# Kernel tuning notes

Hardware: AMD Instinct MI355X
Metric: run time of the kernel (lower is better)

The kernel has to match this reference:

```python
import jax, jax.numpy as jnp
import numpy as np

B, N, C = 2, 10000, 128
NH, NP = 4, 20          # n_heads, n_points (n_levels = 1)
DH = C // NH            # head dim = 32
HW = 100                # spatial shape (100, 100), N = HW*HW


def setup_inputs() -> dict:
    key = jax.random.key(0)
    ks = jax.random.split(key, 12)
    s = 0.05  # small param scale so softmax/linears stay well-conditioned
    return {
        "query": jax.random.normal(ks[0], (B, N, C), jnp.float32),
        "query_pos": jax.random.normal(ks[1], (B, N, C), jnp.float32),
        "W_val": jax.random.normal(ks[2], (C, C), jnp.float32) * s,
        "b_val": jax.random.normal(ks[3], (C,), jnp.float32) * s,
        "W_off": jax.random.normal(ks[4], (NH * NP * 2, C), jnp.float32) * s,
        "b_off": jax.random.normal(ks[5], (NH * NP * 2,), jnp.float32) * s,
        "W_attn": jax.random.normal(ks[6], (NH * NP, C), jnp.float32) * s,
        "b_attn": jax.random.normal(ks[7], (NH * NP,), jnp.float32) * s,
        "W_out1": jax.random.normal(ks[8], (C, C), jnp.float32) * s,
        "b_out1": jax.random.normal(ks[9], (C,), jnp.float32) * s,
        "W_out2": jax.random.normal(ks[10], (C, C), jnp.float32) * s,
        "b_out2": jax.random.normal(ks[11], (C,), jnp.float32) * s,
    }


def _msdeform_forward(query, query_pos, W_val, b_val, W_off, b_off,
                      W_attn, b_attn, W_out1, b_out1, W_out2, b_out2):
    residual = query
    q = query + query_pos  # pos added; value branch also uses q (query.clone())

    # reference points: meshgrid of (z, x) normalized to (0,1), shape (N, 2)
    lin = (jnp.arange(HW, dtype=jnp.float32) + 0.5) / HW
    ref_z, ref_x = jnp.meshgrid(lin, lin, indexing="ij")
    ref = jnp.stack([ref_z.reshape(-1), ref_x.reshape(-1)], axis=-1)  # (N,2)

    # projections
    value = (q @ W_val.T + b_val).reshape(B, N, NH, DH).transpose(0, 2, 1, 3)  # (B,NH,N,DH)
    off = (q @ W_off.T + b_off).reshape(B, N, NH, NP, 2)
    attn = jax.nn.softmax((q @ W_attn.T + b_attn).reshape(B, N, NH, NP), axis=-1)

    # sampling locations in normalized coords; offset normalizer = (W, H) = (100, 100)
    loc = ref[None, :, None, None, :] + off / HW  # (B,N,NH,NP,2)

    # grid_sample bilinear, align_corners=False, zeros padding:
    # pixel coord = loc * size - 0.5
    x = (loc[..., 0] * HW - 0.5).transpose(0, 2, 1, 3)  # (B,NH,N,NP)
    y = (loc[..., 1] * HW - 0.5).transpose(0, 2, 1, 3)
    aw = attn.transpose(0, 2, 1, 3)                     # (B,NH,N,NP)

    x0f = jnp.floor(x); y0f = jnp.floor(y)
    wx1 = x - x0f; wy1 = y - y0f
    wx0 = 1.0 - wx1; wy0 = 1.0 - wy1
    ix0 = x0f.astype(jnp.int32); iy0 = y0f.astype(jnp.int32)
    ix1 = ix0 + 1; iy1 = iy0 + 1

    def gather(ix, iy):
        valid = ((ix >= 0) & (ix < HW) & (iy >= 0) & (iy < HW)).astype(value.dtype)
        idx = jnp.clip(iy, 0, HW - 1) * HW + jnp.clip(ix, 0, HW - 1)  # (B,NH,N,NP)
        g = jnp.take_along_axis(value, idx.reshape(B, NH, N * NP, 1), axis=2)
        return g.reshape(B, NH, N, NP, DH) * valid[..., None]

    sampled = ((wx0 * wy0)[..., None] * gather(ix0, iy0)
               + (wx1 * wy0)[..., None] * gather(ix1, iy0)
               + (wx0 * wy1)[..., None] * gather(ix0, iy1)
               + (wx1 * wy1)[..., None] * gather(ix1, iy1))  # (B,NH,N,NP,DH)

    out = (sampled * aw[..., None]).sum(axis=3)             # (B,NH,N,DH)
    out = out.transpose(0, 2, 1, 3).reshape(B, N, C)
    out = out @ W_out1.T + b_out1   # MSDeformAttn.output_proj
    out = out @ W_out2.T + b_out2   # wrapper output_proj
    return out + residual           # dropout is identity in eval


def reference(query, query_pos, W_val, b_val, W_off, b_off,
              W_attn, b_attn, W_out1, b_out1, W_out2, b_out2):
    return _msdeform_forward(query, query_pos, W_val, b_val, W_off, b_off,
                             W_attn, b_attn, W_out1, b_out1, W_out2, b_out2)
```

## Files before the change

kernel.cpp:

```cpp
#include <hip/hip_runtime.h>
#include <hip/hip_bf16.h>
#include <math.h>

#define NTOK 10000
#define BATCH 2
#define CDIM 128
#define NHEAD 4
#define NPNT 20
#define DHEAD 32
#define HWDIM 100
#define MROWS (BATCH * NTOK)
#define OCAT 368
#define OPAD 384
#define PTOK 8
#define PHALO 4
#define PDIM 16
#define NPATCH 13
#define CELLPAD 40

typedef __attribute__((ext_vector_type(8))) short short8v;
typedef __attribute__((ext_vector_type(4))) short short4v;
typedef __attribute__((ext_vector_type(4))) float f32x4;

__device__ __forceinline__ float asf(unsigned u) {
  union { unsigned u; float f; } c; c.u = u; return c.f;
}

__device__ __forceinline__ void acc_cell(const __hip_bfloat16* p, float w,
                                         f32x4& a0, f32x4& a1) {
  int4 u = *(const int4*)p;
  f32x4 g0, g1;
  g0.x = asf(((unsigned)u.x) << 16); g0.y = asf(((unsigned)u.x) & 0xFFFF0000u);
  g0.z = asf(((unsigned)u.y) << 16); g0.w = asf(((unsigned)u.y) & 0xFFFF0000u);
  g1.x = asf(((unsigned)u.z) << 16); g1.y = asf(((unsigned)u.z) & 0xFFFF0000u);
  g1.z = asf(((unsigned)u.w) << 16); g1.w = asf(((unsigned)u.w) & 0xFFFF0000u);
  a0 += g0 * w;
  a1 += g1 * w;
}

__global__ __launch_bounds__(128) void prep_kernel(
    const float* __restrict__ W_val, const float* __restrict__ b_val,
    const float* __restrict__ W_off, const float* __restrict__ b_off,
    const float* __restrict__ W_attn, const float* __restrict__ b_attn,
    const float* __restrict__ W1, const float* __restrict__ b1,
    const float* __restrict__ W2, const float* __restrict__ b2,
    __hip_bfloat16* __restrict__ Wcat, float* __restrict__ bcat,
    __hip_bfloat16* __restrict__ Wc_bf, float* __restrict__ bc) {
  __shared__ float w2row[128];
  __shared__ float red[128];
  const int blk = blockIdx.x, c = threadIdx.x;
  if (blk < OPAD) {
    float v = 0.f, bv = 0.f;
    if (blk < 128) { v = W_val[blk * 128 + c]; bv = b_val[blk]; }
    else if (blk < 288) { v = W_off[(blk - 128) * 128 + c]; bv = b_off[blk - 128]; }
    else if (blk < OCAT) { v = W_attn[(blk - 288) * 128 + c]; bv = b_attn[blk - 288]; }
    Wcat[(size_t)blk * 128 + c] = __float2bfloat16(v);
    if (c == 0) bcat[blk] = bv;
  } else {
    const int o = blk - OPAD;
    w2row[c] = W2[o * 128 + c];
    __syncthreads();
    float acc = 0.f;
    for (int k = 0; k < 128; ++k) acc += w2row[k] * W1[k * 128 + c];
    Wc_bf[(size_t)o * 128 + c] = __float2bfloat16(acc);
    red[c] = w2row[c] * b1[c];
    __syncthreads();
    for (int s = 64; s > 0; s >>= 1) {
      if (c < s) red[c] += red[c + s];
      __syncthreads();
    }
    if (c == 0) bc[o] = b2[o] + red[0];
  }
}

template <int MODE, int AKIND>
__global__ __launch_bounds__(256) void mfma_proj_kernel(
    const float* __restrict__ src_f, const float* __restrict__ src2,
    const __hip_bfloat16* __restrict__ src_b,
    const __hip_bfloat16* __restrict__ Wb, const float* __restrict__ bias,
    __hip_bfloat16* __restrict__ value, __hip_bfloat16* __restrict__ offo,
    float* __restrict__ attno, float* __restrict__ out,
    const float* __restrict__ resid, int M, int Otiles, int Ototal) {
  __shared__ __hip_bfloat16 qa[64][128];
  __shared__ __hip_bfloat16 wb[64][128];
  const int t = threadIdx.x;
  const int r0 = blockIdx.x * 64;

#pragma unroll
  for (int i = 0; i < 4; ++i) {
    int lin = t + 256 * i;
    int r = lin >> 4;
    int g = lin & 15;
    if (AKIND == 0) {
      int c = g << 3;
      float4 v0 = make_float4(0.f, 0.f, 0.f, 0.f);
      float4 v1 = make_float4(0.f, 0.f, 0.f, 0.f);
      if (r0 + r < M) {
        const float* p = src_f + (size_t)(r0 + r) * CDIM + c;
        v0 = *(const float4*)p;
        v1 = *(const float4*)(p + 4);
        const float* p2 = src2 + (size_t)(r0 + r) * CDIM + c;
        float4 u0 = *(const float4*)p2;
        float4 u1 = *(const float4*)(p2 + 4);
        v0.x += u0.x; v0.y += u0.y; v0.z += u0.z; v0.w += u0.w;
        v1.x += u1.x; v1.y += u1.y; v1.z += u1.z; v1.w += u1.w;
      }
      __hip_bfloat16* dst = &qa[r][(g ^ (r & 7)) << 3];
      dst[0] = __float2bfloat16(v0.x); dst[1] = __float2bfloat16(v0.y);
      dst[2] = __float2bfloat16(v0.z); dst[3] = __float2bfloat16(v0.w);
      dst[4] = __float2bfloat16(v1.x); dst[5] = __float2bfloat16(v1.y);
      dst[6] = __float2bfloat16(v1.z); dst[7] = __float2bfloat16(v1.w);
    } else {
      short8v v = (short8v)(short)0;
      if (r0 + r < M)
        v = *(const short8v*)(src_b + (size_t)(r0 + r) * CDIM + (g << 3));
      *(short8v*)&qa[r][(g ^ (r & 7)) << 3] = v;
    }
  }
  __syncthreads();

  const int wid = t >> 6;
  const int lane = t & 63;
  const int wr = (wid >> 1) * 32;
  const int wc = (wid & 1) * 32;
  const int lrow = lane & 15;
  const int lk = lane >> 4;

  short8v afr[4][2];
  {
    int ra0 = wr + lrow, ra1 = wr + 16 + lrow;
#pragma unroll
    for (int kk = 0; kk < 4; ++kk) {
      int gb = kk * 4 + lk;
      afr[kk][0] = *(const short8v*)&qa[ra0][(gb ^ (ra0 & 7)) << 3];
      afr[kk][1] = *(const short8v*)&qa[ra1][(gb ^ (ra1 & 7)) << 3];
    }
  }

  for (int ti = 0; ti < Otiles; ++ti) {
    const int ot = (blockIdx.y * Otiles + ti) * 64;
    __syncthreads();
#pragma unroll
    for (int i = 0; i < 4; ++i) {
      int lin = t + 256 * i;
      int r = lin >> 4;
      int g = lin & 15;
      short8v w = *(const short8v*)(Wb + (size_t)(ot + r) * 128 + (g << 3));
      *(short8v*)&wb[r][(g ^ (r & 7)) << 3] = w;
    }
    __syncthreads();

    f32x4 acc[2][2];
#pragma unroll
    for (int mi = 0; mi < 2; ++mi)
#pragma unroll
      for (int ni = 0; ni < 2; ++ni) acc[mi][ni] = (f32x4)(0.f);

#pragma unroll
    for (int kk = 0; kk < 4; ++kk) {
      const int gb = kk * 4 + lk;
      int rb0 = wc + lrow, rb1 = wc + 16 + lrow;
      short8v b0 = *(const short8v*)&wb[rb0][(gb ^ (rb0 & 7)) << 3];
      short8v b1 = *(const short8v*)&wb[rb1][(gb ^ (rb1 & 7)) << 3];
      acc[0][0] = __builtin_amdgcn_mfma_f32_16x16x32_bf16(afr[kk][0], b0, acc[0][0], 0, 0, 0);
      acc[0][1] = __builtin_amdgcn_mfma_f32_16x16x32_bf16(afr[kk][0], b1, acc[0][1], 0, 0, 0);
      acc[1][0] = __builtin_amdgcn_mfma_f32_16x16x32_bf16(afr[kk][1], b0, acc[1][0], 0, 0, 0);
      acc[1][1] = __builtin_amdgcn_mfma_f32_16x16x32_bf16(afr[kk][1], b1, acc[1][1], 0, 0, 0);
    }

#pragma unroll
    for (int mi = 0; mi < 2; ++mi) {
#pragma unroll
      for (int ni = 0; ni < 2; ++ni) {
#pragma unroll
        for (int reg = 0; reg < 4; ++reg) {
          int r = r0 + wr + mi * 16 + (lane >> 4) * 4 + reg;
          int o = ot + wc + ni * 16 + (lane & 15);
          if (r >= M || o >= Ototal) continue;
          float v = acc[mi][ni][reg] + bias[o];
          if (MODE == 1) {
            out[(size_t)r * CDIM + o] = v + resid[(size_t)r * CDIM + o];
          } else {
            int b = r >= NTOK ? 1 : 0;
            int n = r - b * NTOK;
            if (o < 128) {
              int h = o >> 5, rem = o & 31;
              value[(((size_t)b * NHEAD + h) * NTOK + n) * 32 + rem] =
                  __float2bfloat16(v);
            } else if (o < 288) {
              int oo = o - 128, h = oo / 40, rem = oo - h * 40;
              offo[(((size_t)b * NHEAD + h) * NTOK + n) * 40 + rem] =
                  __float2bfloat16(v);
            } else {
              int oo = o - 288, h = oo / 20, rem = oo - h * 20;
              attno[(((size_t)b * NHEAD + h) * NTOK + n) * 20 + rem] = v;
            }
          }
        }
      }
    }
  }
}

__global__ __launch_bounds__(256) void sample_kernel(
    const __hip_bfloat16* __restrict__ value,
    const __hip_bfloat16* __restrict__ off, const float* __restrict__ attn,
    __hip_bfloat16* __restrict__ outat) {
  const int s = blockIdx.x & 7;
  const int pidx = blockIdx.x >> 3;
  const int PI = pidx % NPATCH, PJ = pidx / NPATCH;
  const int I0 = PI * PTOK, J0 = PJ * PTOK;
  const int b = s >> 2, h = s & 3;

  __shared__ __hip_bfloat16 patch[PDIM * PDIM][CELLPAD];
  const __hip_bfloat16* vglob = value + (size_t)s * NTOK * DHEAD;

#pragma unroll
  for (int it = 0; it < 4; ++it) {
    int lin = threadIdx.x + 256 * it;
    int cell = lin >> 2, part = lin & 3;
    int py = cell >> 4, px = cell & 15;
    int gy = J0 - PHALO + py;
    int gx = I0 - PHALO + px;
    short8v v = (short8v)(short)0;
    if (gy >= 0 && gy < HWDIM && gx >= 0 && gx < HWDIM)
      v = *(const short8v*)(vglob + ((size_t)(gy * HWDIM + gx)) * DHEAD +
                            part * 8);
    *(short8v*)&patch[cell][part * 8] = v;
  }
  __syncthreads();

  const int dl = threadIdx.x & 3;
  const int tok = threadIdx.x >> 2;
  const int li = tok & 7, lj = tok >> 3;
  const int i = I0 + li, j = J0 + lj;
  if (i >= HWDIM || j >= HWDIM) return;
  const int n = i * HWDIM + j;

  union { int4 v4[5]; unsigned u[20]; } of;
  union { float4 v4[5]; float f[20]; } at;
  {
    const int4* o4 = (const int4*)(off + ((size_t)s * NTOK + n) * 40);
    const float4* a4 = (const float4*)(attn + ((size_t)s * NTOK + n) * 20);
#pragma unroll
    for (int q = 0; q < 5; ++q) of.v4[q] = o4[q];
#pragma unroll
    for (int q = 0; q < 5; ++q) at.v4[q] = a4[q];
  }

  float ssum = 0.f;
#pragma unroll
  for (int p = 0; p < NPNT; ++p) {
    at.f[p] = __expf(at.f[p]);
    ssum += at.f[p];
  }
  const float inv = 1.f / ssum;

  const float fi = (float)i, fj = (float)j;
  f32x4 c0a = (f32x4)(0.f), c0b = (f32x4)(0.f);
  f32x4 c1a = (f32x4)(0.f), c1b = (f32x4)(0.f);
  f32x4 c2a = (f32x4)(0.f), c2b = (f32x4)(0.f);
  f32x4 c3a = (f32x4)(0.f), c3b = (f32x4)(0.f);
#pragma unroll
  for (int p = 0; p < NPNT; ++p) {
    const unsigned up = of.u[p];
    float x = fi + asf(up << 16);
    float y = fj + asf(up & 0xFFFF0000u);
    float aw = at.f[p];
    float x0f = floorf(x), y0f = floorf(y);
    int ix0 = (int)x0f, iy0 = (int)y0f;
    float wx1 = x - x0f, wy1 = y - y0f;
    float wx0 = 1.f - wx1, wy0 = 1.f - wy1;
    float wya = aw * wy0, wyb = aw * wy1;
    float w00 = wya * wx0, w01 = wya * wx1;
    float w10 = wyb * wx0, w11 = wyb * wx1;
    int ly = iy0 - (J0 - PHALO);
    int lx = ix0 - (I0 - PHALO);
    if (ly >= 0 && ly <= PDIM - 2 && lx >= 0 && lx <= PDIM - 2) {
      const __hip_bfloat16* pb = &patch[ly * PDIM + lx][dl * 8];
      acc_cell(pb, w00, c0a, c0b);
      acc_cell(pb + CELLPAD, w01, c1a, c1b);
      acc_cell(pb + PDIM * CELLPAD, w10, c2a, c2b);
      acc_cell(pb + PDIM * CELLPAD + CELLPAD, w11, c3a, c3b);
    } else {
      float wgt[4] = {w00, w01, w10, w11};
#pragma unroll
      for (int cy = 0; cy < 2; ++cy) {
        int iy = iy0 + cy;
        if (iy < 0 || iy >= HWDIM) continue;
#pragma unroll
        for (int cx = 0; cx < 2; ++cx) {
          int ix = ix0 + cx;
          if (ix < 0 || ix >= HWDIM) continue;
          acc_cell(vglob + ((size_t)(iy * HWDIM + ix)) * DHEAD + dl * 8,
                   wgt[cy * 2 + cx], c0a, c0b);
        }
      }
    }
  }
  f32x4 a0 = (c0a + c1a) + (c2a + c3a);
  f32x4 a1 = (c0b + c1b) + (c2b + c3b);

  union { short8v v8; __hip_bfloat16 hh[8]; } o;
#pragma unroll
  for (int k = 0; k < 4; ++k) {
    o.hh[k] = __float2bfloat16(a0[k] * inv);
    o.hh[4 + k] = __float2bfloat16(a1[k] * inv);
  }
  *(short8v*)(outat + ((size_t)b * NTOK + n) * CDIM + h * DHEAD + dl * 8) =
      o.v8;
}

extern "C" void kernel_launch(void* const* d_in, const int* in_sizes, int n_in,
                              void* d_out, int out_size, void* d_ws,
                              size_t ws_size, hipStream_t stream) {
  const float* query = (const float*)d_in[0];
  const float* query_pos = (const float*)d_in[1];
  const float* W_val = (const float*)d_in[2];
  const float* b_val = (const float*)d_in[3];
  const float* W_off = (const float*)d_in[4];
  const float* b_off = (const float*)d_in[5];
  const float* W_attn = (const float*)d_in[6];
  const float* b_attn = (const float*)d_in[7];
  const float* W_out1 = (const float*)d_in[8];
  const float* b_out1 = (const float*)d_in[9];
  const float* W_out2 = (const float*)d_in[10];
  const float* b_out2 = (const float*)d_in[11];
  float* out = (float*)d_out;

  char* ws = (char*)d_ws;
  __hip_bfloat16* value = (__hip_bfloat16*)ws;
  ws += (size_t)MROWS * CDIM * 2;
  __hip_bfloat16* offb = (__hip_bfloat16*)ws;
  ws += (size_t)MROWS * 160 * 2;
  float* attnb = (float*)ws;
  ws += (size_t)MROWS * 80 * 4;
  __hip_bfloat16* outat = (__hip_bfloat16*)ws;
  ws += (size_t)MROWS * CDIM * 2;
  float* bc = (float*)ws; ws += 128 * 4;
  float* bcat = (float*)ws; ws += OPAD * 4;
  __hip_bfloat16* Wcat = (__hip_bfloat16*)ws; ws += (size_t)OPAD * 128 * 2;
  __hip_bfloat16* Wc_bf = (__hip_bfloat16*)ws;

  prep_kernel<<<OPAD + 128, 128, 0, stream>>>(
      W_val, b_val, W_off, b_off, W_attn, b_attn, W_out1, b_out1, W_out2,
      b_out2, Wcat, bcat, Wc_bf, bc);

  mfma_proj_kernel<0, 0><<<dim3(313, 2), 256, 0, stream>>>(
      query, query_pos, nullptr, Wcat, bcat, value, offb, attnb, nullptr,
      nullptr, MROWS, 3, OCAT);

  sample_kernel<<<8 * NPATCH * NPATCH, 256, 0, stream>>>(value, offb, attnb,
                                                         outat);

  mfma_proj_kernel<1, 1><<<dim3(313, 2), 256, 0, stream>>>(
      nullptr, nullptr, outat, Wc_bf, bc, nullptr, nullptr, nullptr, out,
      query, MROWS, 1, 128);
}
```

Before: 60.73 us.

## Drop weight-prep kernel, convert weights inline, chain output projections in one kernel

Removes the separate prep kernel that pre-converted weights to bf16 and folded the two output linears into one. Each projection kernel now loads the fp32 weights and converts them in shared memory, using 512-thread blocks that cover 128 output columns per tile. The second kernel runs both output linears back to back with the intermediate kept in LDS. This saves a launch and the workspace round trip, at the cost of redoing the weight conversion in every block and running two GEMMs instead of one folded GEMM. The sample kernel also issues its offset and attention loads before the patch fill.

New measurement: 70.23 us. 15.6% more time.

```diff
diff --git a/kernel.cpp b/kernel.cpp
--- a/kernel.cpp
+++ b/kernel.cpp
@@ -11,7 +11,6 @@
 #define HWDIM 100
 #define MROWS (BATCH * NTOK)
 #define OCAT 368
-#define OPAD 384
 #define PTOK 8
 #define PHALO 4
 #define PDIM 16
@@ -38,91 +37,51 @@
   a1 += g1 * w;
 }
 
-__global__ __launch_bounds__(128) void prep_kernel(
+__device__ __forceinline__ void cvt8_store(__hip_bfloat16* dst, float4 v0,
+                                           float4 v1) {
+  dst[0] = __float2bfloat16(v0.x); dst[1] = __float2bfloat16(v0.y);
+  dst[2] = __float2bfloat16(v0.z); dst[3] = __float2bfloat16(v0.w);
+  dst[4] = __float2bfloat16(v1.x); dst[5] = __float2bfloat16(v1.y);
+  dst[6] = __float2bfloat16(v1.z); dst[7] = __float2bfloat16(v1.w);
+}
+
+__global__ __launch_bounds__(512) void proj1_kernel(
+    const float* __restrict__ query, const float* __restrict__ qpos,
     const float* __restrict__ W_val, const float* __restrict__ b_val,
     const float* __restrict__ W_off, const float* __restrict__ b_off,
     const float* __restrict__ W_attn, const float* __restrict__ b_attn,
-    const float* __restrict__ W1, const float* __restrict__ b1,
-    const float* __restrict__ W2, const float* __restrict__ b2,
-    __hip_bfloat16* __restrict__ Wcat, float* __restrict__ bcat,
-    __hip_bfloat16* __restrict__ Wc_bf, float* __restrict__ bc) {
-  __shared__ float w2row[128];
-  __shared__ float red[128];
-  const int blk = blockIdx.x, c = threadIdx.x;
-  if (blk < OPAD) {
-    float v = 0.f, bv = 0.f;
-    if (blk < 128) { v = W_val[blk * 128 + c]; bv = b_val[blk]; }
-    else if (blk < 288) { v = W_off[(blk - 128) * 128 + c]; bv = b_off[blk - 128]; }
-    else if (blk < OCAT) { v = W_attn[(blk - 288) * 128 + c]; bv = b_attn[blk - 288]; }
-    Wcat[(size_t)blk * 128 + c] = __float2bfloat16(v);
-    if (c == 0) bcat[blk] = bv;
-  } else {
-    const int o = blk - OPAD;
-    w2row[c] = W2[o * 128 + c];
-    __syncthreads();
-    float acc = 0.f;
-    for (int k = 0; k < 128; ++k) acc += w2row[k] * W1[k * 128 + c];
-    Wc_bf[(size_t)o * 128 + c] = __float2bfloat16(acc);
-    red[c] = w2row[c] * b1[c];
-    __syncthreads();
-    for (int s = 64; s > 0; s >>= 1) {
-      if (c < s) red[c] += red[c + s];
-      __syncthreads();
-    }
-    if (c == 0) bc[o] = b2[o] + red[0];
-  }
-}
-
-template <int MODE, int AKIND>
-__global__ __launch_bounds__(256) void mfma_proj_kernel(
-    const float* __restrict__ src_f, const float* __restrict__ src2,
-    const __hip_bfloat16* __restrict__ src_b,
-    const __hip_bfloat16* __restrict__ Wb, const float* __restrict__ bias,
     __hip_bfloat16* __restrict__ value, __hip_bfloat16* __restrict__ offo,
-    float* __restrict__ attno, float* __restrict__ out,
-    const float* __restrict__ resid, int M, int Otiles, int Ototal) {
+    float* __restrict__ attno) {
   __shared__ __hip_bfloat16 qa[64][128];
-  __shared__ __hip_bfloat16 wb[64][128];
+  __shared__ __hip_bfloat16 wb[128][128];
   const int t = threadIdx.x;
   const int r0 = blockIdx.x * 64;
 
 #pragma unroll
-  for (int i = 0; i < 4; ++i) {
-    int lin = t + 256 * i;
-    int r = lin >> 4;
-    int g = lin & 15;
-    if (AKIND == 0) {
-      int c = g << 3;
-      float4 v0 = make_float4(0.f, 0.f, 0.f, 0.f);
-      float4 v1 = make_float4(0.f, 0.f, 0.f, 0.f);
-      if (r0 + r < M) {
-        const float* p = src_f + (size_t)(r0 + r) * CDIM + c;
-        v0 = *(const float4*)p;
-        v1 = *(const float4*)(p + 4);
-        const float* p2 = src2 + (size_t)(r0 + r) * CDIM + c;
-        float4 u0 = *(const float4*)p2;
-        float4 u1 = *(const float4*)(p2 + 4);
-        v0.x += u0.x; v0.y += u0.y; v0.z += u0.z; v0.w += u0.w;
-        v1.x += u1.x; v1.y += u1.y; v1.z += u1.z; v1.w += u1.w;
-      }
-      __hip_bfloat16* dst = &qa[r][(g ^ (r & 7)) << 3];
-      dst[0] = __float2bfloat16(v0.x); dst[1] = __float2bfloat16(v0.y);
-      dst[2] = __float2bfloat16(v0.z); dst[3] = __float2bfloat16(v0.w);
-      dst[4] = __float2bfloat16(v1.x); dst[5] = __float2bfloat16(v1.y);
-      dst[6] = __float2bfloat16(v1.z); dst[7] = __float2bfloat16(v1.w);
-    } else {
-      short8v v = (short8v)(short)0;
-      if (r0 + r < M)
-        v = *(const short8v*)(src_b + (size_t)(r0 + r) * CDIM + (g << 3));
-      *(short8v*)&qa[r][(g ^ (r & 7)) << 3] = v;
-    }
+  for (int i = 0; i < 2; ++i) {
+    int lin = t + 512 * i;
+    int r = lin >> 4, g = lin & 15;
+    int c = g << 3;
+    float4 v0 = make_float4(0.f, 0.f, 0.f, 0.f);
+    float4 v1 = make_float4(0.f, 0.f, 0.f, 0.f);
+    if (r0 + r < MROWS) {
+      const float* p = query + (size_t)(r0 + r) * CDIM + c;
+      v0 = *(const float4*)p;
+      v1 = *(const float4*)(p + 4);
+      const float* p2 = qpos + (size_t)(r0 + r) * CDIM + c;
+      float4 u0 = *(const float4*)p2;
+      float4 u1 = *(const float4*)(p2 + 4);
+      v0.x += u0.x; v0.y += u0.y; v0.z += u0.z; v0.w += u0.w;
+      v1.x += u1.x; v1.y += u1.y; v1.z += u1.z; v1.w += u1.w;
+    }
+    cvt8_store(&qa[r][(g ^ (r & 7)) << 3], v0, v1);
   }
   __syncthreads();
 
   const int wid = t >> 6;
   const int lane = t & 63;
-  const int wr = (wid >> 1) * 32;
-  const int wc = (wid & 1) * 32;
+  const int wr = (wid >> 2) * 32;
+  const int wc = (wid & 3) * 32;
   const int lrow = lane & 15;
   const int lk = lane >> 4;
 
@@ -137,16 +96,26 @@
     }
   }
 
-  for (int ti = 0; ti < Otiles; ++ti) {
-    const int ot = (blockIdx.y * Otiles + ti) * 64;
+  for (int ti = 0; ti < 3; ++ti) {
+    const int ot = ti * 128;
     __syncthreads();
 #pragma unroll
     for (int i = 0; i < 4; ++i) {
-      int lin = t + 256 * i;
+      int lin = t + 512 * i;
       int r = lin >> 4;
       int g = lin & 15;
-      short8v w = *(const short8v*)(Wb + (size_t)(ot + r) * 128 + (g << 3));
-      *(short8v*)&wb[r][(g ^ (r & 7)) << 3] = w;
+      int grow = ot + r;
+      float4 w0 = make_float4(0.f, 0.f, 0.f, 0.f);
+      float4 w1 = make_float4(0.f, 0.f, 0.f, 0.f);
+      if (grow < OCAT) {
+        const float* src;
+        if (grow < 128) src = W_val + (size_t)grow * 128;
+        else if (grow < 288) src = W_off + (size_t)(grow - 128) * 128;
+        else src = W_attn + (size_t)(grow - 288) * 128;
+        w0 = *(const float4*)(src + (g << 3));
+        w1 = *(const float4*)(src + (g << 3) + 4);
+      }
+      cvt8_store(&wb[r][(g ^ (r & 7)) << 3], w0, w1);
     }
     __syncthreads();
 
@@ -176,27 +145,160 @@
         for (int reg = 0; reg < 4; ++reg) {
           int r = r0 + wr + mi * 16 + (lane >> 4) * 4 + reg;
           int o = ot + wc + ni * 16 + (lane & 15);
-          if (r >= M || o >= Ototal) continue;
-          float v = acc[mi][ni][reg] + bias[o];
-          if (MODE == 1) {
-            out[(size_t)r * CDIM + o] = v + resid[(size_t)r * CDIM + o];
+          if (r >= MROWS || o >= OCAT) continue;
+          float bv;
+          if (o < 128) bv = b_val[o];
+          else if (o < 288) bv = b_off[o - 128];
+          else bv = b_attn[o - 288];
+          float v = acc[mi][ni][reg] + bv;
+          int b = r >= NTOK ? 1 : 0;
+          int n = r - b * NTOK;
+          if (o < 128) {
+            int h = o >> 5, rem = o & 31;
+            value[(((size_t)b * NHEAD + h) * NTOK + n) * 32 + rem] =
+                __float2bfloat16(v);
+          } else if (o < 288) {
+            int oo = o - 128, h = oo / 40, rem = oo - h * 40;
+            offo[(((size_t)b * NHEAD + h) * NTOK + n) * 40 + rem] =
+                __float2bfloat16(v);
           } else {
-            int b = r >= NTOK ? 1 : 0;
-            int n = r - b * NTOK;
-            if (o < 128) {
-              int h = o >> 5, rem = o & 31;
-              value[(((size_t)b * NHEAD + h) * NTOK + n) * 32 + rem] =
-                  __float2bfloat16(v);
-            } else if (o < 288) {
-              int oo = o - 128, h = oo / 40, rem = oo - h * 40;
-              offo[(((size_t)b * NHEAD + h) * NTOK + n) * 40 + rem] =
-                  __float2bfloat16(v);
-            } else {
-              int oo = o - 288, h = oo / 20, rem = oo - h * 20;
-              attno[(((size_t)b * NHEAD + h) * NTOK + n) * 20 + rem] = v;
-            }
+            int oo = o - 288, h = oo / 20, rem = oo - h * 20;
+            attno[(((size_t)b * NHEAD + h) * NTOK + n) * 20 + rem] = v;
           }
         }
+      }
+    }
+  }
+}
+
+__global__ __launch_bounds__(512) void proj2_kernel(
+    const __hip_bfloat16* __restrict__ outat, const float* __restrict__ W1,
+    const float* __restrict__ b1, const float* __restrict__ W2,
+    const float* __restrict__ b2, const float* __restrict__ resid,
+    float* __restrict__ out) {
+  __shared__ __hip_bfloat16 qa[64][128];
+  __shared__ __hip_bfloat16 wb[128][128];
+  const int t = threadIdx.x;
+  const int r0 = blockIdx.x * 64;
+
+#pragma unroll
+  for (int i = 0; i < 2; ++i) {
+    int lin = t + 512 * i;
+    int r = lin >> 4, g = lin & 15;
+    short8v v = (short8v)(short)0;
+    if (r0 + r < MROWS)
+      v = *(const short8v*)(outat + (size_t)(r0 + r) * CDIM + (g << 3));
+    *(short8v*)&qa[r][(g ^ (r & 7)) << 3] = v;
+  }
+  __syncthreads();
+
+  const int wid = t >> 6;
+  const int lane = t & 63;
+  const int wr = (wid >> 2) * 32;
+  const int wc = (wid & 3) * 32;
+  const int lrow = lane & 15;
+  const int lk = lane >> 4;
+
+  short8v afr[4][2];
+  {
+    int ra0 = wr + lrow, ra1 = wr + 16 + lrow;
+#pragma unroll
+    for (int kk = 0; kk < 4; ++kk) {
+      int gb = kk * 4 + lk;
+      afr[kk][0] = *(const short8v*)&qa[ra0][(gb ^ (ra0 & 7)) << 3];
+      afr[kk][1] = *(const short8v*)&qa[ra1][(gb ^ (ra1 & 7)) << 3];
+    }
+  }
+
+#pragma unroll
+  for (int i = 0; i < 4; ++i) {
+    int lin = t + 512 * i;
+    int r = lin >> 4, g = lin & 15;
+    const float* src = W1 + (size_t)r * 128;
+    float4 w0 = *(const float4*)(src + (g << 3));
+    float4 w1 = *(const float4*)(src + (g << 3) + 4);
+    cvt8_store(&wb[r][(g ^ (r & 7)) << 3], w0, w1);
+  }
+  __syncthreads();
+
+  f32x4 acc[2][2];
+#pragma unroll
+  for (int mi = 0; mi < 2; ++mi)
+#pragma unroll
+    for (int ni = 0; ni < 2; ++ni) acc[mi][ni] = (f32x4)(0.f);
+#pragma unroll
+  for (int kk = 0; kk < 4; ++kk) {
+    const int gb = kk * 4 + lk;
+    int rb0 = wc + lrow, rb1 = wc + 16 + lrow;
+    short8v b0 = *(const short8v*)&wb[rb0][(gb ^ (rb0 & 7)) << 3];
+    short8v b1v = *(const short8v*)&wb[rb1][(gb ^ (rb1 & 7)) << 3];
+    acc[0][0] = __builtin_amdgcn_mfma_f32_16x16x32_bf16(afr[kk][0], b0, acc[0][0], 0, 0, 0);
+    acc[0][1] = __builtin_amdgcn_mfma_f32_16x16x32_bf16(afr[kk][0], b1v, acc[0][1], 0, 0, 0);
+    acc[1][0] = __builtin_amdgcn_mfma_f32_16x16x32_bf16(afr[kk][1], b0, acc[1][0], 0, 0, 0);
+    acc[1][1] = __builtin_amdgcn_mfma_f32_16x16x32_bf16(afr[kk][1], b1v, acc[1][1], 0, 0, 0);
+  }
+#pragma unroll
+  for (int mi = 0; mi < 2; ++mi) {
+#pragma unroll
+    for (int ni = 0; ni < 2; ++ni) {
+#pragma unroll
+      for (int reg = 0; reg < 4; ++reg) {
+        int r = wr + mi * 16 + (lane >> 4) * 4 + reg;
+        int o = wc + ni * 16 + (lane & 15);
+        float v = acc[mi][ni][reg] + b1[o];
+        qa[r][((o >> 3) ^ (r & 7)) * 8 + (o & 7)] = __float2bfloat16(v);
+      }
+    }
+  }
+  __syncthreads();
+
+  short8v afr2[4][2];
+  {
+    int ra0 = wr + lrow, ra1 = wr + 16 + lrow;
+#pragma unroll
+    for (int kk = 0; kk < 4; ++kk) {
+      int gb = kk * 4 + lk;
+      afr2[kk][0] = *(const short8v*)&qa[ra0][(gb ^ (ra0 & 7)) << 3];
+      afr2[kk][1] = *(const short8v*)&qa[ra1][(gb ^ (ra1 & 7)) << 3];
+    }
+  }
+#pragma unroll
+  for (int i = 0; i < 4; ++i) {
+    int lin = t + 512 * i;
+    int r = lin >> 4, g = lin & 15;
+    const float* src = W2 + (size_t)r * 128;
+    float4 w0 = *(const float4*)(src + (g << 3));
+    float4 w1 = *(const float4*)(src + (g << 3) + 4);
+    cvt8_store(&wb[r][(g ^ (r & 7)) << 3], w0, w1);
+  }
+  __syncthreads();
+
+#pragma unroll
+  for (int mi = 0; mi < 2; ++mi)
+#pragma unroll
+    for (int ni = 0; ni < 2; ++ni) acc[mi][ni] = (f32x4)(0.f);
+#pragma unroll
+  for (int kk = 0; kk < 4; ++kk) {
+    const int gb = kk * 4 + lk;
+    int rb0 = wc + lrow, rb1 = wc + 16 + lrow;
+    short8v b0 = *(const short8v*)&wb[rb0][(gb ^ (rb0 & 7)) << 3];
+    short8v b1v = *(const short8v*)&wb[rb1][(gb ^ (rb1 & 7)) << 3];
+    acc[0][0] = __builtin_amdgcn_mfma_f32_16x16x32_bf16(afr2[kk][0], b0, acc[0][0], 0, 0, 0);
+    acc[0][1] = __builtin_amdgcn_mfma_f32_16x16x32_bf16(afr2[kk][0], b1v, acc[0][1], 0, 0, 0);
+    acc[1][0] = __builtin_amdgcn_mfma_f32_16x16x32_bf16(afr2[kk][1], b0, acc[1][0], 0, 0, 0);
+    acc[1][1] = __builtin_amdgcn_mfma_f32_16x16x32_bf16(afr2[kk][1], b1v, acc[1][1], 0, 0, 0);
+  }
+#pragma unroll
+  for (int mi = 0; mi < 2; ++mi) {
+#pragma unroll
+    for (int ni = 0; ni < 2; ++ni) {
+#pragma unroll
+      for (int reg = 0; reg < 4; ++reg) {
+        int r = r0 + wr + mi * 16 + (lane >> 4) * 4 + reg;
+        int o = wc + ni * 16 + (lane & 15);
+        if (r >= MROWS) continue;
+        out[(size_t)r * CDIM + o] =
+            acc[mi][ni][reg] + b2[o] + resid[(size_t)r * CDIM + o];
       }
     }
   }
@@ -214,6 +316,23 @@
 
   __shared__ __hip_bfloat16 patch[PDIM * PDIM][CELLPAD];
   const __hip_bfloat16* vglob = value + (size_t)s * NTOK * DHEAD;
+
+  const int dl = threadIdx.x & 3;
+  const int tok = threadIdx.x >> 2;
+  const int li = tok & 7, lj = tok >> 3;
+  const int i = I0 + li, j = J0 + lj;
+  const bool tv = (i < HWDIM) && (j < HWDIM);
+  const int n = tv ? (i * HWDIM + j) : 0;
+  union { int4 v4[5]; unsigned u[20]; } of;
+  union { float4 v4[5]; float f[20]; } at;
+  {
+    const int4* o4 = (const int4*)(off + ((size_t)s * NTOK + n) * 40);
+    const float4* a4 = (const float4*)(attn + ((size_t)s * NTOK + n) * 20);
+#pragma unroll
+    for (int q = 0; q < 5; ++q) of.v4[q] = o4[q];
+#pragma unroll
+    for (int q = 0; q < 5; ++q) at.v4[q] = a4[q];
+  }
 
 #pragma unroll
   for (int it = 0; it < 4; ++it) {
@@ -230,23 +349,7 @@
   }
   __syncthreads();
 
-  const int dl = threadIdx.x & 3;
-  const int tok = threadIdx.x >> 2;
-  const int li = tok & 7, lj = tok >> 3;
-  const int i = I0 + li, j = J0 + lj;
-  if (i >= HWDIM || j >= HWDIM) return;
-  const int n = i * HWDIM + j;
-
-  union { int4 v4[5]; unsigned u[20]; } of;
-  union { float4 v4[5]; float f[20]; } at;
-  {
-    const int4* o4 = (const int4*)(off + ((size_t)s * NTOK + n) * 40);
-    const float4* a4 = (const float4*)(attn + ((size_t)s * NTOK + n) * 20);
-#pragma unroll
-    for (int q = 0; q < 5; ++q) of.v4[q] = o4[q];
-#pragma unroll
-    for (int q = 0; q < 5; ++q) at.v4[q] = a4[q];
-  }
+  if (!tv) return;
 
   float ssum = 0.f;
 #pragma unroll
@@ -276,7 +379,7 @@
     float w10 = wyb * wx0, w11 = wyb * wx1;
     int ly = iy0 - (J0 - PHALO);
     int lx = ix0 - (I0 - PHALO);
-    if (ly >= 0 && ly <= PDIM - 2 && lx >= 0 && lx <= PDIM - 2) {
+    if ((unsigned)ly <= PDIM - 2 && (unsigned)lx <= PDIM - 2) {
       const __hip_bfloat16* pb = &patch[ly * PDIM + lx][dl * 8];
       acc_cell(pb, w00, c0a, c0b);
       acc_cell(pb + CELLPAD, w01, c1a, c1b);
@@ -336,24 +439,14 @@
   float* attnb = (float*)ws;
   ws += (size_t)MROWS * 80 * 4;
   __hip_bfloat16* outat = (__hip_bfloat16*)ws;
-  ws += (size_t)MROWS * CDIM * 2;
-  float* bc = (float*)ws; ws += 128 * 4;
-  float* bcat = (float*)ws; ws += OPAD * 4;
-  __hip_bfloat16* Wcat = (__hip_bfloat16*)ws; ws += (size_t)OPAD * 128 * 2;
-  __hip_bfloat16* Wc_bf = (__hip_bfloat16*)ws;
-
-  prep_kernel<<<OPAD + 128, 128, 0, stream>>>(
-      W_val, b_val, W_off, b_off, W_attn, b_attn, W_out1, b_out1, W_out2,
-      b_out2, Wcat, bcat, Wc_bf, bc);
-
-  mfma_proj_kernel<0, 0><<<dim3(313, 2), 256, 0, stream>>>(
-      query, query_pos, nullptr, Wcat, bcat, value, offb, attnb, nullptr,
-      nullptr, MROWS, 3, OCAT);
+
+  proj1_kernel<<<313, 512, 0, stream>>>(query, query_pos, W_val, b_val, W_off,
+                                        b_off, W_attn, b_attn, value, offb,
+                                        attnb);
 
   sample_kernel<<<8 * NPATCH * NPATCH, 256, 0, stream>>>(value, offb, attnb,
                                                          outat);
 
-  mfma_proj_kernel<1, 1><<<dim3(313, 2), 256, 0, stream>>>(
-      nullptr, nullptr, outat, Wc_bf, bc, nullptr, nullptr, nullptr, out,
-      query, MROWS, 1, 128);
-}
+  proj2_kernel<<<313, 512, 0, stream>>>(outat, W_out1, b_out1, W_out2, b_out2,
+                                        query, out);
+}
```

## Interleave offset/attn outputs per head, prefetch weight tiles, specialize projection kernels

Applied to the files above, without the earlier changes.

Reorders the concatenated offset and attention weights so that each head owns a 64-wide slot (40 offsets, 20 logits, 4 pad). The first projection then writes one token-major bf16 buffer that the sampler reads with eight contiguous 16-byte loads, in place of separate head-major offset and fp32 attention buffers. The projection GEMM is split into two specialized kernels, and the first one prefetches the next weight tile into registers while the current tile's MFMAs run. Attention logits are now stored in bf16, which loses some precision before the softmax.

Result: faster. 58.91 us (-3.0%).

```diff
diff --git a/kernel.cpp b/kernel.cpp
--- a/kernel.cpp
+++ b/kernel.cpp
@@ -10,7 +10,6 @@
 #define DHEAD 32
 #define HWDIM 100
 #define MROWS (BATCH * NTOK)
-#define OCAT 368
 #define OPAD 384
 #define PTOK 8
 #define PHALO 4
@@ -51,9 +50,13 @@
   const int blk = blockIdx.x, c = threadIdx.x;
   if (blk < OPAD) {
     float v = 0.f, bv = 0.f;
-    if (blk < 128) { v = W_val[blk * 128 + c]; bv = b_val[blk]; }
-    else if (blk < 288) { v = W_off[(blk - 128) * 128 + c]; bv = b_off[blk - 128]; }
-    else if (blk < OCAT) { v = W_attn[(blk - 288) * 128 + c]; bv = b_attn[blk - 288]; }
+    if (blk < 128) {
+      v = W_val[blk * 128 + c]; bv = b_val[blk];
+    } else {
+      int h = (blk - 128) >> 6, k = (blk - 128) & 63;
+      if (k < 40) { v = W_off[(h * 40 + k) * 128 + c]; bv = b_off[h * 40 + k]; }
+      else if (k < 60) { v = W_attn[(h * 20 + k - 40) * 128 + c]; bv = b_attn[h * 20 + k - 40]; }
+    }
     Wcat[(size_t)blk * 128 + c] = __float2bfloat16(v);
     if (c == 0) bcat[blk] = bv;
   } else {
@@ -73,14 +76,10 @@
   }
 }
 
-template <int MODE, int AKIND>
-__global__ __launch_bounds__(256) void mfma_proj_kernel(
-    const float* __restrict__ src_f, const float* __restrict__ src2,
-    const __hip_bfloat16* __restrict__ src_b,
-    const __hip_bfloat16* __restrict__ Wb, const float* __restrict__ bias,
-    __hip_bfloat16* __restrict__ value, __hip_bfloat16* __restrict__ offo,
-    float* __restrict__ attno, float* __restrict__ out,
-    const float* __restrict__ resid, int M, int Otiles, int Ototal) {
+__global__ __launch_bounds__(256) void proj1_kernel(
+    const float* __restrict__ query, const float* __restrict__ qpos,
+    const __hip_bfloat16* __restrict__ Wcat, const float* __restrict__ bcat,
+    __hip_bfloat16* __restrict__ value, __hip_bfloat16* __restrict__ oa) {
   __shared__ __hip_bfloat16 qa[64][128];
   __shared__ __hip_bfloat16 wb[64][128];
   const int t = threadIdx.x;
@@ -89,32 +88,34 @@
 #pragma unroll
   for (int i = 0; i < 4; ++i) {
     int lin = t + 256 * i;
-    int r = lin >> 4;
-    int g = lin & 15;
-    if (AKIND == 0) {
-      int c = g << 3;
-      float4 v0 = make_float4(0.f, 0.f, 0.f, 0.f);
-      float4 v1 = make_float4(0.f, 0.f, 0.f, 0.f);
-      if (r0 + r < M) {
-        const float* p = src_f + (size_t)(r0 + r) * CDIM + c;
-        v0 = *(const float4*)p;
-        v1 = *(const float4*)(p + 4);
-        const float* p2 = src2 + (size_t)(r0 + r) * CDIM + c;
-        float4 u0 = *(const float4*)p2;
-        float4 u1 = *(const float4*)(p2 + 4);
-        v0.x += u0.x; v0.y += u0.y; v0.z += u0.z; v0.w += u0.w;
-        v1.x += u1.x; v1.y += u1.y; v1.z += u1.z; v1.w += u1.w;
-      }
-      __hip_bfloat16* dst = &qa[r][(g ^ (r & 7)) << 3];
-      dst[0] = __float2bfloat16(v0.x); dst[1] = __float2bfloat16(v0.y);
-      dst[2] = __float2bfloat16(v0.z); dst[3] = __float2bfloat16(v0.w);
-      dst[4] = __float2bfloat16(v1.x); dst[5] = __float2bfloat16(v1.y);
-      dst[6] = __float2bfloat16(v1.z); dst[7] = __float2bfloat16(v1.w);
-    } else {
-      short8v v = (short8v)(short)0;
-      if (r0 + r < M)
-        v = *(const short8v*)(src_b + (size_t)(r0 + r) * CDIM + (g << 3));
-      *(short8v*)&qa[r][(g ^ (r & 7)) << 3] = v;
+    int r = lin >> 4, g = lin & 15;
+    int c = g << 3;
+    float4 v0 = make_float4(0.f, 0.f, 0.f, 0.f);
+    float4 v1 = make_float4(0.f, 0.f, 0.f, 0.f);
+    if (r0 + r < MROWS) {
+      const float* p = query + (size_t)(r0 + r) * CDIM + c;
+      v0 = *(const float4*)p;
+      v1 = *(const float4*)(p + 4);
+      const float* p2 = qpos + (size_t)(r0 + r) * CDIM + c;
+      float4 u0 = *(const float4*)p2;
+      float4 u1 = *(const float4*)(p2 + 4);
+      v0.x += u0.x; v0.y += u0.y; v0.z += u0.z; v0.w += u0.w;
+      v1.x += u1.x; v1.y += u1.y; v1.z += u1.z; v1.w += u1.w;
+    }
+    __hip_bfloat16* dst = &qa[r][(g ^ (r & 7)) << 3];
+    dst[0] = __float2bfloat16(v0.x); dst[1] = __float2bfloat16(v0.y);
+    dst[2] = __float2bfloat16(v0.z); dst[3] = __float2bfloat16(v0.w);
+    dst[4] = __float2bfloat16(v1.x); dst[5] = __float2bfloat16(v1.y);
+    dst[6] = __float2bfloat16(v1.z); dst[7] = __float2bfloat16(v1.w);
+  }
+  {
+    const int ot = blockIdx.y * 192;
+#pragma unroll
+    for (int i = 0; i < 4; ++i) {
+      int lin = t + 256 * i;
+      int r = lin >> 4, g = lin & 15;
+      short8v w = *(const short8v*)(Wcat + (size_t)(ot + r) * 128 + (g << 3));
+      *(short8v*)&wb[r][(g ^ (r & 7)) << 3] = w;
     }
   }
   __syncthreads();
@@ -137,18 +138,20 @@
     }
   }
 
-  for (int ti = 0; ti < Otiles; ++ti) {
-    const int ot = (blockIdx.y * Otiles + ti) * 64;
-    __syncthreads();
-#pragma unroll
-    for (int i = 0; i < 4; ++i) {
-      int lin = t + 256 * i;
-      int r = lin >> 4;
-      int g = lin & 15;
-      short8v w = *(const short8v*)(Wb + (size_t)(ot + r) * 128 + (g << 3));
-      *(short8v*)&wb[r][(g ^ (r & 7)) << 3] = w;
-    }
-    __syncthreads();
+#pragma unroll
+  for (int ti = 0; ti < 3; ++ti) {
+    const int ot = blockIdx.y * 192 + ti * 64;
+
+    short8v wreg[4];
+    if (ti < 2) {
+      const int otn = ot + 64;
+#pragma unroll
+      for (int i = 0; i < 4; ++i) {
+        int lin = t + 256 * i;
+        int r = lin >> 4, g = lin & 15;
+        wreg[i] = *(const short8v*)(Wcat + (size_t)(otn + r) * 128 + (g << 3));
+      }
+    }
 
     f32x4 acc[2][2];
 #pragma unroll
@@ -168,6 +171,16 @@
       acc[1][1] = __builtin_amdgcn_mfma_f32_16x16x32_bf16(afr[kk][1], b1, acc[1][1], 0, 0, 0);
     }
 
+    if (ti < 2) {
+      __syncthreads();
+#pragma unroll
+      for (int i = 0; i < 4; ++i) {
+        int lin = t + 256 * i;
+        int r = lin >> 4, g = lin & 15;
+        *(short8v*)&wb[r][(g ^ (r & 7)) << 3] = wreg[i];
+      }
+    }
+
 #pragma unroll
     for (int mi = 0; mi < 2; ++mi) {
 #pragma unroll
@@ -176,36 +189,100 @@
         for (int reg = 0; reg < 4; ++reg) {
           int r = r0 + wr + mi * 16 + (lane >> 4) * 4 + reg;
           int o = ot + wc + ni * 16 + (lane & 15);
-          if (r >= M || o >= Ototal) continue;
-          float v = acc[mi][ni][reg] + bias[o];
-          if (MODE == 1) {
-            out[(size_t)r * CDIM + o] = v + resid[(size_t)r * CDIM + o];
-          } else {
+          if (r >= MROWS) continue;
+          float v = acc[mi][ni][reg] + bcat[o];
+          if (o < 128) {
             int b = r >= NTOK ? 1 : 0;
             int n = r - b * NTOK;
-            if (o < 128) {
-              int h = o >> 5, rem = o & 31;
-              value[(((size_t)b * NHEAD + h) * NTOK + n) * 32 + rem] =
-                  __float2bfloat16(v);
-            } else if (o < 288) {
-              int oo = o - 128, h = oo / 40, rem = oo - h * 40;
-              offo[(((size_t)b * NHEAD + h) * NTOK + n) * 40 + rem] =
-                  __float2bfloat16(v);
-            } else {
-              int oo = o - 288, h = oo / 20, rem = oo - h * 20;
-              attno[(((size_t)b * NHEAD + h) * NTOK + n) * 20 + rem] = v;
-            }
+            int h = o >> 5, rem = o & 31;
+            value[(((size_t)b * NHEAD + h) * NTOK + n) * 32 + rem] =
+                __float2bfloat16(v);
+          } else {
+            oa[(size_t)r * 256 + (o - 128)] = __float2bfloat16(v);
           }
         }
       }
     }
+
+    if (ti < 2) __syncthreads();
+  }
+}
+
+__global__ __launch_bounds__(256) void proj2_kernel(
+    const __hip_bfloat16* __restrict__ outat,
+    const __hip_bfloat16* __restrict__ Wc_bf, const float* __restrict__ bc,
+    const float* __restrict__ resid, float* __restrict__ out) {
+  __shared__ __hip_bfloat16 qa[64][128];
+  __shared__ __hip_bfloat16 wb[64][128];
+  const int t = threadIdx.x;
+  const int r0 = blockIdx.x * 64;
+  const int ot = blockIdx.y * 64;
+
+#pragma unroll
+  for (int i = 0; i < 4; ++i) {
+    int lin = t + 256 * i;
+    int r = lin >> 4, g = lin & 15;
+    short8v v = (short8v)(short)0;
+    if (r0 + r < MROWS)
+      v = *(const short8v*)(outat + (size_t)(r0 + r) * CDIM + (g << 3));
+    *(short8v*)&qa[r][(g ^ (r & 7)) << 3] = v;
+  }
+#pragma unroll
+  for (int i = 0; i < 4; ++i) {
+    int lin = t + 256 * i;
+    int r = lin >> 4, g = lin & 15;
+    short8v w = *(const short8v*)(Wc_bf + (size_t)(ot + r) * 128 + (g << 3));
+    *(short8v*)&wb[r][(g ^ (r & 7)) << 3] = w;
+  }
+  __syncthreads();
+
+  const int wid = t >> 6;
+  const int lane = t & 63;
+  const int wr = (wid >> 1) * 32;
+  const int wc = (wid & 1) * 32;
+  const int lrow = lane & 15;
+  const int lk = lane >> 4;
+
+  f32x4 acc[2][2];
+#pragma unroll
+  for (int mi = 0; mi < 2; ++mi)
+#pragma unroll
+    for (int ni = 0; ni < 2; ++ni) acc[mi][ni] = (f32x4)(0.f);
+
+#pragma unroll
+  for (int kk = 0; kk < 4; ++kk) {
+    const int gb = kk * 4 + lk;
+    int ra0 = wr + lrow, ra1 = wr + 16 + lrow;
+    int rb0 = wc + lrow, rb1 = wc + 16 + lrow;
+    short8v a0 = *(const short8v*)&qa[ra0][(gb ^ (ra0 & 7)) << 3];
+    short8v a1 = *(const short8v*)&qa[ra1][(gb ^ (ra1 & 7)) << 3];
+    short8v b0 = *(const short8v*)&wb[rb0][(gb ^ (rb0 & 7)) << 3];
+    short8v b1 = *(const short8v*)&wb[rb1][(gb ^ (rb1 & 7)) << 3];
+    acc[0][0] = __builtin_amdgcn_mfma_f32_16x16x32_bf16(a0, b0, acc[0][0], 0, 0, 0);
+    acc[0][1] = __builtin_amdgcn_mfma_f32_16x16x32_bf16(a0, b1, acc[0][1], 0, 0, 0);
+    acc[1][0] = __builtin_amdgcn_mfma_f32_16x16x32_bf16(a1, b0, acc[1][0], 0, 0, 0);
+    acc[1][1] = __builtin_amdgcn_mfma_f32_16x16x32_bf16(a1, b1, acc[1][1], 0, 0, 0);
+  }
+
+#pragma unroll
+  for (int mi = 0; mi < 2; ++mi) {
+#pragma unroll
+    for (int ni = 0; ni < 2; ++ni) {
+#pragma unroll
+      for (int reg = 0; reg < 4; ++reg) {
+        int r = r0 + wr + mi * 16 + (lane >> 4) * 4 + reg;
+        int o = ot + wc + ni * 16 + (lane & 15);
+        if (r >= MROWS) continue;
+        out[(size_t)r * CDIM + o] =
+            acc[mi][ni][reg] + bc[o] + resid[(size_t)r * CDIM + o];
+      }
+    }
   }
 }
 
 __global__ __launch_bounds__(256) void sample_kernel(
     const __hip_bfloat16* __restrict__ value,
-    const __hip_bfloat16* __restrict__ off, const float* __restrict__ attn,
-    __hip_bfloat16* __restrict__ outat) {
+    const __hip_bfloat16* __restrict__ oa, __hip_bfloat16* __restrict__ outat) {
   const int s = blockIdx.x & 7;
   const int pidx = blockIdx.x >> 3;
   const int PI = pidx % NPATCH, PJ = pidx / NPATCH;
@@ -237,22 +314,23 @@
   if (i >= HWDIM || j >= HWDIM) return;
   const int n = i * HWDIM + j;
 
-  union { int4 v4[5]; unsigned u[20]; } of;
-  union { float4 v4[5]; float f[20]; } at;
+  union { int4 v4[8]; unsigned u[32]; } d;
   {
-    const int4* o4 = (const int4*)(off + ((size_t)s * NTOK + n) * 40);
-    const float4* a4 = (const float4*)(attn + ((size_t)s * NTOK + n) * 20);
-#pragma unroll
-    for (int q = 0; q < 5; ++q) of.v4[q] = o4[q];
-#pragma unroll
-    for (int q = 0; q < 5; ++q) at.v4[q] = a4[q];
-  }
-
+    const int4* p4 =
+        (const int4*)(oa + ((size_t)(b * NTOK + n)) * 256 + h * 64);
+#pragma unroll
+    for (int q = 0; q < 8; ++q) d.v4[q] = p4[q];
+  }
+
+  float e[NPNT];
   float ssum = 0.f;
 #pragma unroll
-  for (int p = 0; p < NPNT; ++p) {
-    at.f[p] = __expf(at.f[p]);
-    ssum += at.f[p];
+  for (int q = 0; q < 10; ++q) {
+    unsigned uu = d.u[20 + q];
+    float e0 = __expf(asf(uu << 16));
+    float e1 = __expf(asf(uu & 0xFFFF0000u));
+    e[2 * q] = e0; e[2 * q + 1] = e1;
+    ssum += e0 + e1;
   }
   const float inv = 1.f / ssum;
 
@@ -263,10 +341,10 @@
   f32x4 c3a = (f32x4)(0.f), c3b = (f32x4)(0.f);
 #pragma unroll
   for (int p = 0; p < NPNT; ++p) {
-    const unsigned up = of.u[p];
+    const unsigned up = d.u[p];
     float x = fi + asf(up << 16);
     float y = fj + asf(up & 0xFFFF0000u);
-    float aw = at.f[p];
+    float aw = e[p];
     float x0f = floorf(x), y0f = floorf(y);
     int ix0 = (int)x0f, iy0 = (int)y0f;
     float wx1 = x - x0f, wy1 = y - y0f;
@@ -276,7 +354,7 @@
     float w10 = wyb * wx0, w11 = wyb * wx1;
     int ly = iy0 - (J0 - PHALO);
     int lx = ix0 - (I0 - PHALO);
-    if (ly >= 0 && ly <= PDIM - 2 && lx >= 0 && lx <= PDIM - 2) {
+    if ((unsigned)ly <= PDIM - 2 && (unsigned)lx <= PDIM - 2) {
       const __hip_bfloat16* pb = &patch[ly * PDIM + lx][dl * 8];
       acc_cell(pb, w00, c0a, c0b);
       acc_cell(pb + CELLPAD, w01, c1a, c1b);
@@ -331,14 +409,12 @@
   char* ws = (char*)d_ws;
   __hip_bfloat16* value = (__hip_bfloat16*)ws;
   ws += (size_t)MROWS * CDIM * 2;
-  __hip_bfloat16* offb = (__hip_bfloat16*)ws;
-  ws += (size_t)MROWS * 160 * 2;
-  float* attnb = (float*)ws;
-  ws += (size_t)MROWS * 80 * 4;
+  __hip_bfloat16* oa = (__hip_bfloat16*)ws;
+  ws += (size_t)MROWS * 256 * 2;
   __hip_bfloat16* outat = (__hip_bfloat16*)ws;
   ws += (size_t)MROWS * CDIM * 2;
+  float* bcat = (float*)ws; ws += OPAD * 4;
   float* bc = (float*)ws; ws += 128 * 4;
-  float* bcat = (float*)ws; ws += OPAD * 4;
   __hip_bfloat16* Wcat = (__hip_bfloat16*)ws; ws += (size_t)OPAD * 128 * 2;
   __hip_bfloat16* Wc_bf = (__hip_bfloat16*)ws;
 
@@ -346,14 +422,10 @@
       W_val, b_val, W_off, b_off, W_attn, b_attn, W_out1, b_out1, W_out2,
       b_out2, Wcat, bcat, Wc_bf, bc);
 
-  mfma_proj_kernel<0, 0><<<dim3(313, 2), 256, 0, stream>>>(
-      query, query_pos, nullptr, Wcat, bcat, value, offb, attnb, nullptr,
-      nullptr, MROWS, 3, OCAT);
-
-  sample_kernel<<<8 * NPATCH * NPATCH, 256, 0, stream>>>(value, offb, attnb,
-                                                         outat);
-
-  mfma_proj_kernel<1, 1><<<dim3(313, 2), 256, 0, stream>>>(
-      nullptr, nullptr, outat, Wc_bf, bc, nullptr, nullptr, nullptr, out,
-      query, MROWS, 1, 128);
-}
+  proj1_kernel<<<dim3(313, 2), 256, 0, stream>>>(query, query_pos, Wcat, bcat,
+                                                 value, oa);
+
+  sample_kernel<<<8 * NPATCH * NPATCH, 256, 0, stream>>>(value, oa, outat);
+
+  proj2_kernel<<<dim3(313, 2), 256, 0, stream>>>(outat, Wc_bf, bc, query, out);
+}
```
